# Kernel tuning notes

Hardware: AMD Instinct MI355X
Metric: run time of the kernel (lower is better)

## Reference

```python
import jax, jax.numpy as jnp
import numpy as np

C = 512  # n_channels

def _maxpool2x2(t):
    # t: [B, C, H, W] -> [B, C, H//2, W//2]
    B, Cc, H, W = t.shape
    return t.reshape(B, Cc, H // 2, 2, W // 2, 2).max(axis=(3, 5))

def setup_inputs() -> dict:
    key = jax.random.key(0)
    ks = jax.random.split(key, 6)
    B, H, W = 16, 64, 64
    x = jax.random.normal(ks[0], (B, C, H, W), dtype=jnp.float32)
    # 1x1 conv weights (spectral-normalized convs, no bias) stored as [out, in]
    wq = jax.random.normal(ks[1], (C // 8, C), dtype=jnp.float32) * 0.05
    wk = jax.random.normal(ks[2], (C // 8, C), dtype=jnp.float32) * 0.05
    wv = jax.random.normal(ks[3], (C // 2, C), dtype=jnp.float32) * 0.05
    wo = jax.random.normal(ks[4], (C, C // 2), dtype=jnp.float32) * 0.05
    gamma = jnp.zeros((1,), dtype=jnp.float32) + 0.5  # nonzero so output depends on attention path
    return {"x": x, "wq": wq, "wk": wk, "wv": wv, "wo": wo, "gamma": gamma}

def reference(x, wq, wk, wv, wo, gamma):
    B, Cc, H, W = x.shape
    n = H * W
    # 1x1 convs are channel-mixing matmuls
    f = jnp.einsum('oc,bchw->bohw', wq, x).reshape(B, Cc // 8, n)            # [B, C/8, n]
    g = _maxpool2x2(jnp.einsum('oc,bchw->bohw', wk, x)).reshape(B, Cc // 8, n // 4)  # [B, C/8, n/4]
    h = _maxpool2x2(jnp.einsum('oc,bchw->bohw', wv, x)).reshape(B, Cc // 2, n // 4)  # [B, C/2, n/4]
    # attention: softmax over pooled kv positions
    beta = jax.nn.softmax(jnp.einsum('bcn,bcm->bnm', f, g), axis=-1)         # [B, n, n/4]
    o = jnp.einsum('bcm,bnm->bcn', h, beta).reshape(B, Cc // 2, H, W)        # [B, C/2, H, W]
    o = jnp.einsum('oc,bchw->bohw', wo, o)                                   # [B, C, H, W]
    return gamma.reshape(()) * o + x
```

## Files before the change

kernel.cpp:

```cpp
#include <hip/hip_runtime.h>
#include <cstdint>
#include <cstddef>

namespace {

constexpr int kB  = 16;
constexpr int kC  = 512;
constexpr int kCQ = 64;
constexpr int kCV = 256;
constexpr int kN  = 4096;
constexpr int kM  = 1024;

typedef _Float16 f16;
typedef _Float16 f16x8 __attribute__((ext_vector_type(8)));
typedef float    f32x4 __attribute__((ext_vector_type(4)));

__global__ __launch_bounds__(256)
void convert_weights_kernel(const float* __restrict__ wq,
                            const float* __restrict__ wk,
                            const float* __restrict__ wv,
                            const float* __restrict__ wo,
                            const float* __restrict__ gamma,
                            f16* __restrict__ wcat,
                            f16* __restrict__ woh)
{
    const int idx = blockIdx.x * 256 + threadIdx.x;
    if (idx < 49152) {
        const int e = idx * 4;
        const int r = e >> 9, c = e & 511;
        const float* src = (r < 64)  ? (wq + ((size_t)r << 9))
                         : (r < 128) ? (wk + ((size_t)(r - 64) << 9))
                                     : (wv + ((size_t)(r - 128) << 9));
        float4 v = *(const float4*)(src + c);
        union { f16 h4[4]; uint2 u; } pk;
        pk.h4[0] = (f16)v.x;
        pk.h4[1] = (f16)v.y;
        pk.h4[2] = (f16)v.z;
        pk.h4[3] = (f16)v.w;
        *(uint2*)(wcat + e) = pk.u;
    } else {
        const int e = (idx - 49152) * 4;
        const float g = gamma[0];
        float4 v = *(const float4*)(wo + e);
        union { f16 h4[4]; uint2 u; } pk;
        pk.h4[0] = (f16)(g * v.x);
        pk.h4[1] = (f16)(g * v.y);
        pk.h4[2] = (f16)(g * v.z);
        pk.h4[3] = (f16)(g * v.w);
        *(uint2*)(woh + e) = pk.u;
    }
}

__global__ __launch_bounds__(512, 2)
void proj_pool_mfma(const float* __restrict__ x,
                    const f16* __restrict__ wcat,
                    f16* __restrict__ fT,
                    f16* __restrict__ gT,
                    f16* __restrict__ h)
{
    const int nt  = blockIdx.x;
    const int b   = blockIdx.y;
    const int tid = threadIdx.x;
    const int w    = tid >> 6;
    const int lane = tid & 63;
    const int quad = lane >> 4;
    const int lq   = lane & 15;
    const int wr   = w >> 1;
    const int wc   = w & 1;

    __shared__ alignas(16) f16 As[384 * 40];
    __shared__ alignas(16) f16 Bs[128 * 40];

    const float* Xb = x + (size_t)b * kC * kN + nt * 128;

    f32x4 acc[6][4];
#pragma unroll
    for (int i = 0; i < 6; ++i)
#pragma unroll
        for (int j = 0; j < 4; ++j) acc[i][j] = {0.f, 0.f, 0.f, 0.f};

    const int bn = tid & 127;
    const int kg = tid >> 7;

    uint4 pa[3];
    float xv[8];
#pragma unroll
    for (int p = 0; p < 3; ++p) {
        const int unit = tid + p * 512;
        const int row = unit >> 2, su = unit & 3;
        pa[p] = *(const uint4*)(wcat + (size_t)row * kC + su * 8);
    }
#pragma unroll
    for (int j = 0; j < 8; ++j) xv[j] = Xb[(size_t)(kg * 8 + j) * kN + bn];

    for (int ks = 0; ks < 16; ++ks) {
        __syncthreads();
#pragma unroll
        for (int p = 0; p < 3; ++p) {
            const int unit = tid + p * 512;
            const int row = unit >> 2, su = unit & 3;
            *(uint4*)&As[row * 40 + su * 8] = pa[p];
        }
        {
            union { f16 hh[8]; uint4 u; } pk;
#pragma unroll
            for (int j = 0; j < 8; ++j) pk.hh[j] = (f16)xv[j];
            *(uint4*)&Bs[bn * 40 + kg * 8] = pk.u;
        }
        __syncthreads();
        if (ks < 15) {
            const int k0 = (ks + 1) * 32;
#pragma unroll
            for (int p = 0; p < 3; ++p) {
                const int unit = tid + p * 512;
                const int row = unit >> 2, su = unit & 3;
                pa[p] = *(const uint4*)(wcat + (size_t)row * kC + k0 + su * 8);
            }
#pragma unroll
            for (int j = 0; j < 8; ++j)
                xv[j] = Xb[(size_t)(k0 + kg * 8 + j) * kN + bn];
        }

        f16x8 bsv[4];
#pragma unroll
        for (int tj = 0; tj < 4; ++tj) {
            const int col = (tj < 2) ? (wc * 32 + tj * 16 + lq)
                                     : (64 + wc * 32 + (tj - 2) * 16 + lq);
            bsv[tj] = *(const f16x8*)&Bs[col * 40 + quad * 8];
        }
        __builtin_amdgcn_s_setprio(1);
#pragma unroll
        for (int ti = 0; ti < 6; ++ti) {
            const f16x8 af = *(const f16x8*)&As[(wr * 96 + ti * 16 + lq) * 40 + quad * 8];
#pragma unroll
            for (int tj = 0; tj < 4; ++tj)
                acc[ti][tj] = __builtin_amdgcn_mfma_f32_16x16x32_f16(
                    af, bsv[tj], acc[ti][tj], 0, 0, 0);
        }
        __builtin_amdgcn_s_setprio(0);
    }

#pragma unroll
    for (int ti = 0; ti < 6; ++ti) {
        const int ch0 = wr * 96 + ti * 16;
        if (ch0 < 64) {
            f16* fb = fT + (size_t)b * kN * kCQ;
#pragma unroll
            for (int tj = 0; tj < 4; ++tj) {
                const int col = (tj < 2) ? (wc * 32 + tj * 16 + lq)
                                         : (64 + wc * 32 + (tj - 2) * 16 + lq);
                const int n = nt * 128 + col;
                union { f16 h4[4]; uint2 u; } pk;
#pragma unroll
                for (int r = 0; r < 4; ++r) pk.h4[r] = (f16)acc[ti][tj][r];
                *(uint2*)(fb + (size_t)n * kCQ + ch0 + quad * 4) = pk.u;
            }
        } else {
#pragma unroll
            for (int tjp = 0; tjp < 2; ++tjp) {
                float p[4];
#pragma unroll
                for (int r = 0; r < 4; ++r) {
                    float v = fmaxf(acc[ti][tjp][r], acc[ti][tjp + 2][r]);
                    v = fmaxf(v, __shfl_xor(v, 1, 64));
                    p[r] = v;
                }
                const int m = nt * 32 + wc * 16 + tjp * 8 + (lq >> 1);
                if ((lq & 1) == 0) {
                    if (ch0 < 128) {
                        union { f16 h4[4]; uint2 u; } pk;
#pragma unroll
                        for (int r = 0; r < 4; ++r) pk.h4[r] = (f16)p[r];
                        *(uint2*)(gT + ((size_t)b * kM + m) * kCQ + (ch0 - 64) + quad * 4) = pk.u;
                    } else {
#pragma unroll
                        for (int r = 0; r < 4; ++r) {
                            const int ch = ch0 - 128 + quad * 4 + r;
                            h[((size_t)b * kCV + ch) * kM + m] = (f16)p[r];
                        }
                    }
                }
            }
        }
    }
}

__global__ __launch_bounds__(256, 2)
void attn_out_kernel(const f16* __restrict__ fT,
                     const f16* __restrict__ gT,
                     const f16* __restrict__ hmat,
                     const f16* __restrict__ woh,
                     const float* __restrict__ x,
                     float* __restrict__ out)
{
    const int qt   = blockIdx.x;
    const int b    = blockIdx.y;
    const int tid  = threadIdx.x;
    const int w    = tid >> 6;
    const int lane = tid & 63;
    const int quad = lane >> 4;
    const int lq   = lane & 15;

    __shared__ union alignas(16) SMem {
        struct {
            f16   fsT[128 * 72];
            f16   gsT[32 * 64];
            f16   hs[256 * 40];
            f16   ps[64 * 40];
        } p1;
        struct {
            f16 osT[64 * 264];
            f16 wos[256 * 40];
        } p2;
    } sm;

    {
        const f16* fb = fT + ((size_t)b * kN + qt * 128) * kCQ;
#pragma unroll
        for (int p = 0; p < 4; ++p) {
            const int unit = tid + p * 256;
            const int q = unit >> 3, u = unit & 7;
            *(uint4*)&sm.p1.fsT[q * 72 + u * 8] = *(const uint4*)(fb + q * 64 + u * 8);
        }
    }
    __syncthreads();

    const f16x8 afA0 = *(const f16x8*)&sm.p1.fsT[(w * 16 + lq) * 72 + quad * 8];
    const f16x8 afA1 = *(const f16x8*)&sm.p1.fsT[(w * 16 + lq) * 72 + 32 + quad * 8];
    const f16x8 afB0 = *(const f16x8*)&sm.p1.fsT[(64 + w * 16 + lq) * 72 + quad * 8];
    const f16x8 afB1 = *(const f16x8*)&sm.p1.fsT[(64 + w * 16 + lq) * 72 + 32 + quad * 8];

    float mA = -3.0e38f, lA = 0.f, mB = -3.0e38f, lB = 0.f;
    f32x4 o_accA[16], o_accB[16];
#pragma unroll
    for (int ci = 0; ci < 16; ++ci) {
        o_accA[ci] = {0.f, 0.f, 0.f, 0.f};
        o_accB[ci] = {0.f, 0.f, 0.f, 0.f};
    }

    const f16* gTb = gT + (size_t)b * kM * kCQ;
    const f16* hb  = hmat + (size_t)b * kCV * kM;

    const int gm = tid >> 3, gsu = tid & 7, ggu = gsu ^ (gm & 7);
    const int hc = tid >> 2, hu = tid & 3;
    uint4 pg, ph[4];
    {
        pg = *(const uint4*)(gTb + (size_t)gm * kCQ + ggu * 8);
#pragma unroll
        for (int p = 0; p < 4; ++p)
            ph[p] = *(const uint4*)(hb + (size_t)(hc + p * 64) * kM + hu * 8);
    }

    for (int mi = 0; mi < 32; ++mi) {
        __syncthreads();
        *(uint4*)&sm.p1.gsT[gm * 64 + gsu * 8] = pg;
#pragma unroll
        for (int p = 0; p < 4; ++p)
            *(uint4*)&sm.p1.hs[(hc + p * 64) * 40 + hu * 8] = ph[p];
        __syncthreads();
        if (mi < 31) {
            const int m1 = (mi + 1) * 32;
            pg = *(const uint4*)(gTb + (size_t)(m1 + gm) * kCQ + ggu * 8);
#pragma unroll
            for (int p = 0; p < 4; ++p)
                ph[p] = *(const uint4*)(hb + (size_t)(hc + p * 64) * kM + m1 + hu * 8);
        }

        const int mr0 = lq, mr1 = 16 + lq;
        const f16x8 bg00 = *(const f16x8*)&sm.p1.gsT[mr0 * 64 + ((quad)     ^ (mr0 & 7)) * 8];
        const f16x8 bg01 = *(const f16x8*)&sm.p1.gsT[mr0 * 64 + ((4 + quad) ^ (mr0 & 7)) * 8];
        const f16x8 bg10 = *(const f16x8*)&sm.p1.gsT[mr1 * 64 + ((quad)     ^ (mr1 & 7)) * 8];
        const f16x8 bg11 = *(const f16x8*)&sm.p1.gsT[mr1 * 64 + ((4 + quad) ^ (mr1 & 7)) * 8];
        f32x4 s0A = {0.f,0.f,0.f,0.f}, s1A = {0.f,0.f,0.f,0.f};
        f32x4 s0B = {0.f,0.f,0.f,0.f}, s1B = {0.f,0.f,0.f,0.f};
        s0A = __builtin_amdgcn_mfma_f32_16x16x32_f16(bg00, afA0, s0A, 0, 0, 0);
        s0A = __builtin_amdgcn_mfma_f32_16x16x32_f16(bg01, afA1, s0A, 0, 0, 0);
        s1A = __builtin_amdgcn_mfma_f32_16x16x32_f16(bg10, afA0, s1A, 0, 0, 0);
        s1A = __builtin_amdgcn_mfma_f32_16x16x32_f16(bg11, afA1, s1A, 0, 0, 0);
        s0B = __builtin_amdgcn_mfma_f32_16x16x32_f16(bg00, afB0, s0B, 0, 0, 0);
        s0B = __builtin_amdgcn_mfma_f32_16x16x32_f16(bg01, afB1, s0B, 0, 0, 0);
        s1B = __builtin_amdgcn_mfma_f32_16x16x32_f16(bg10, afB0, s1B, 0, 0, 0);
        s1B = __builtin_amdgcn_mfma_f32_16x16x32_f16(bg11, afB1, s1B, 0, 0, 0);

        float alA;
        {
            float cm = fmaxf(fmaxf(fmaxf(s0A[0], s0A[1]), fmaxf(s0A[2], s0A[3])),
                             fmaxf(fmaxf(s1A[0], s1A[1]), fmaxf(s1A[2], s1A[3])));
            cm = fmaxf(cm, __shfl_xor(cm, 16, 64));
            cm = fmaxf(cm, __shfl_xor(cm, 32, 64));
            const float nm = fmaxf(mA, cm);
            alA = __expf(mA - nm);
            float e0[4], e1[4];
#pragma unroll
            for (int r = 0; r < 4; ++r) { e0[r] = __expf(s0A[r] - nm); e1[r] = __expf(s1A[r] - nm); }
            float psum = (e0[0]+e0[1])+(e0[2]+e0[3])+(e1[0]+e1[1])+(e1[2]+e1[3]);
            psum += __shfl_xor(psum, 16, 64);
            psum += __shfl_xor(psum, 32, 64);
            mA = nm;
            lA = lA * alA + psum;
            union { f16 h4[4]; uint2 u; } pk0, pk1;
#pragma unroll
            for (int r = 0; r < 4; ++r) { pk0.h4[r] = (f16)e0[r]; pk1.h4[r] = (f16)e1[r]; }
            *(uint2*)&sm.p1.ps[(w * 16 + lq) * 40 + quad * 4]      = pk0.u;
            *(uint2*)&sm.p1.ps[(w * 16 + lq) * 40 + 16 + quad * 4] = pk1.u;
        }
        const f16x8 bpA = *(const f16x8*)&sm.p1.ps[(w * 16 + lq) * 40 + quad * 8];
        __builtin_amdgcn_sched_barrier(0);

        float alB;
        {
            float cm = fmaxf(fmaxf(fmaxf(s0B[0], s0B[1]), fmaxf(s0B[2], s0B[3])),
                             fmaxf(fmaxf(s1B[0], s1B[1]), fmaxf(s1B[2], s1B[3])));
            cm = fmaxf(cm, __shfl_xor(cm, 16, 64));
            cm = fmaxf(cm, __shfl_xor(cm, 32, 64));
            const float nm = fmaxf(mB, cm);
            alB = __expf(mB - nm);
            float e0[4], e1[4];
#pragma unroll
            for (int r = 0; r < 4; ++r) { e0[r] = __expf(s0B[r] - nm); e1[r] = __expf(s1B[r] - nm); }
            float psum = (e0[0]+e0[1])+(e0[2]+e0[3])+(e1[0]+e1[1])+(e1[2]+e1[3]);
            psum += __shfl_xor(psum, 16, 64);
            psum += __shfl_xor(psum, 32, 64);
            mB = nm;
            lB = lB * alB + psum;
            union { f16 h4[4]; uint2 u; } pk0, pk1;
#pragma unroll
            for (int r = 0; r < 4; ++r) { pk0.h4[r] = (f16)e0[r]; pk1.h4[r] = (f16)e1[r]; }
            *(uint2*)&sm.p1.ps[(w * 16 + lq) * 40 + quad * 4]      = pk0.u;
            *(uint2*)&sm.p1.ps[(w * 16 + lq) * 40 + 16 + quad * 4] = pk1.u;
        }
        const f16x8 bpB = *(const f16x8*)&sm.p1.ps[(w * 16 + lq) * 40 + quad * 8];
        __builtin_amdgcn_sched_barrier(0);

        __builtin_amdgcn_s_setprio(1);
#pragma unroll
        for (int ci = 0; ci < 16; ++ci) {
            const f16x8 ha = *(const f16x8*)&sm.p1.hs[(ci * 16 + lq) * 40 + quad * 8];
            o_accA[ci] *= alA;
            o_accA[ci] = __builtin_amdgcn_mfma_f32_16x16x32_f16(ha, bpA, o_accA[ci], 0, 0, 0);
            o_accB[ci] *= alB;
            o_accB[ci] = __builtin_amdgcn_mfma_f32_16x16x32_f16(ha, bpB, o_accB[ci], 0, 0, 0);
        }
        __builtin_amdgcn_s_setprio(0);
    }

    const float invA = 1.0f / lA;
    const float invB = 1.0f / lB;

    const int woc = tid >> 2, wu = tid & 3;
    uint4 pw[4];
#pragma unroll
    for (int p = 0; p < 4; ++p)
        pw[p] = *(const uint4*)(woh + (size_t)(woc + p * 64) * 256 + wu * 8);

    __syncthreads();

#pragma unroll
    for (int ci = 0; ci < 16; ++ci) {
        union { f16 h4[4]; uint2 u; } pk;
#pragma unroll
        for (int r = 0; r < 4; ++r) pk.h4[r] = (f16)(o_accA[ci][r] * invA);
        *(uint2*)&sm.p2.osT[(w * 16 + lq) * 264 + ci * 16 + quad * 4] = pk.u;
    }

    int s = 0;
    for (int tile = 0; tile < 2; ++tile) {
        for (int half = 0; half < 2; ++half) {
            f32x4 acc2[16];
#pragma unroll
            for (int os = 0; os < 16; ++os) acc2[os] = {0.f, 0.f, 0.f, 0.f};

            for (int ck = 0; ck < 8; ++ck) {
                __syncthreads();
#pragma unroll
                for (int p = 0; p < 4; ++p)
                    *(uint4*)&sm.p2.wos[(woc + p * 64) * 40 + wu * 8] = pw[p];
                __syncthreads();
                ++s;
                if (s < 32) {
                    const int sp = s & 15;
#pragma unroll
                    for (int p = 0; p < 4; ++p)
                        pw[p] = *(const uint4*)(woh +
                            (size_t)((sp >> 3) * 256 + woc + p * 64) * 256 +
                            (sp & 7) * 32 + wu * 8);
                }
                const f16x8 bo = *(const f16x8*)&sm.p2.osT[(w * 16 + lq) * 264 + ck * 32 + quad * 8];
                __builtin_amdgcn_s_setprio(1);
#pragma unroll
                for (int os = 0; os < 16; ++os) {
                    const f16x8 wa = *(const f16x8*)&sm.p2.wos[(os * 16 + lq) * 40 + quad * 8];
                    acc2[os] = __builtin_amdgcn_mfma_f32_16x16x32_f16(wa, bo, acc2[os], 0, 0, 0);
                }
                __builtin_amdgcn_s_setprio(0);
            }

            const int n0 = qt * 128 + tile * 64 + w * 16 + lq;
#pragma unroll
            for (int os = 0; os < 16; ++os) {
#pragma unroll
                for (int r = 0; r < 4; ++r) {
                    const int oc = half * 256 + os * 16 + quad * 4 + r;
                    const size_t idx = ((size_t)b * kC + oc) * (size_t)kN + n0;
                    out[idx] = acc2[os][r] + x[idx];
                }
            }
        }
        if (tile == 0) {
#pragma unroll
            for (int ci = 0; ci < 16; ++ci) {
                union { f16 h4[4]; uint2 u; } pk;
#pragma unroll
                for (int r = 0; r < 4; ++r) pk.h4[r] = (f16)(o_accB[ci][r] * invB);
                *(uint2*)&sm.p2.osT[(w * 16 + lq) * 264 + ci * 16 + quad * 4] = pk.u;
            }
        }
    }
}

}

extern "C" void kernel_launch(void* const* d_in, const int* in_sizes, int n_in,
                              void* d_out, int out_size, void* d_ws, size_t ws_size,
                              hipStream_t stream) {
    const float* x     = (const float*)d_in[0];
    const float* wq    = (const float*)d_in[1];
    const float* wk    = (const float*)d_in[2];
    const float* wv    = (const float*)d_in[3];
    const float* wo    = (const float*)d_in[4];
    const float* gamma = (const float*)d_in[5];
    float* out = (float*)d_out;

    f16* fT   = (f16*)d_ws;
    f16* gT   = fT  + (size_t)kB * kN * kCQ;
    f16* hw   = gT  + (size_t)kB * kM * kCQ;
    f16* woh  = hw  + (size_t)kB * kCV * kM;
    f16* wcat = woh + (size_t)kC * kCV;

    hipLaunchKernelGGL(convert_weights_kernel, dim3(320), dim3(256), 0, stream,
                       wq, wk, wv, wo, gamma, wcat, woh);
    hipLaunchKernelGGL(proj_pool_mfma, dim3(32, kB), dim3(512), 0, stream,
                       x, wcat, fT, gT, hw);
    hipLaunchKernelGGL(attn_out_kernel, dim3(32, kB), dim3(256), 0, stream,
                       fT, gT, hw, woh, x, out);
}
```

Baseline: 472.3 us.

## Double-buffer LDS stages and split projection channels across a grid dimension

The projection kernel now splits its 384 output channels into two 192-channel blocks along a new grid dimension. It reads weight fragments straight from global memory into registers instead of through LDS, and double-buffers the X tile so each k-step needs only one barrier. The attention kernel double-buffers the g/h chunks and the output-weight tiles with a two-deep register prefetch, which halves the barriers per iteration. In exchange, the X tile is converted twice (once per channel block), LDS use in the attention kernel grows, and register pressure may rise.

```diff
diff --git a/kernel.cpp b/kernel.cpp
--- a/kernel.cpp
+++ b/kernel.cpp
@@ -33,25 +33,21 @@
                                      : (wv + ((size_t)(r - 128) << 9));
         float4 v = *(const float4*)(src + c);
         union { f16 h4[4]; uint2 u; } pk;
-        pk.h4[0] = (f16)v.x;
-        pk.h4[1] = (f16)v.y;
-        pk.h4[2] = (f16)v.z;
-        pk.h4[3] = (f16)v.w;
+        pk.h4[0] = (f16)v.x; pk.h4[1] = (f16)v.y;
+        pk.h4[2] = (f16)v.z; pk.h4[3] = (f16)v.w;
         *(uint2*)(wcat + e) = pk.u;
     } else {
         const int e = (idx - 49152) * 4;
         const float g = gamma[0];
         float4 v = *(const float4*)(wo + e);
         union { f16 h4[4]; uint2 u; } pk;
-        pk.h4[0] = (f16)(g * v.x);
-        pk.h4[1] = (f16)(g * v.y);
-        pk.h4[2] = (f16)(g * v.z);
-        pk.h4[3] = (f16)(g * v.w);
+        pk.h4[0] = (f16)(g * v.x); pk.h4[1] = (f16)(g * v.y);
+        pk.h4[2] = (f16)(g * v.z); pk.h4[3] = (f16)(g * v.w);
         *(uint2*)(woh + e) = pk.u;
     }
 }
 
-__global__ __launch_bounds__(512, 2)
+__global__ __launch_bounds__(512, 4)
 void proj_pool_mfma(const float* __restrict__ x,
                     const f16* __restrict__ wcat,
                     f16* __restrict__ fT,
@@ -59,7 +55,8 @@
                     f16* __restrict__ h)
 {
     const int nt  = blockIdx.x;
-    const int b   = blockIdx.y;
+    const int mt  = blockIdx.y;
+    const int b   = blockIdx.z;
     const int tid = threadIdx.x;
     const int w    = tid >> 6;
     const int lane = tid & 63;
@@ -68,57 +65,56 @@
     const int wr   = w >> 1;
     const int wc   = w & 1;
 
-    __shared__ alignas(16) f16 As[384 * 40];
-    __shared__ alignas(16) f16 Bs[128 * 40];
-
+    __shared__ alignas(16) f16 Bs[2][128 * 36];
+
+    const f16*   Ab = wcat + (size_t)mt * 192 * kC;
     const float* Xb = x + (size_t)b * kC * kN + nt * 128;
 
-    f32x4 acc[6][4];
-#pragma unroll
-    for (int i = 0; i < 6; ++i)
+    f32x4 acc[3][4];
+#pragma unroll
+    for (int i = 0; i < 3; ++i)
 #pragma unroll
         for (int j = 0; j < 4; ++j) acc[i][j] = {0.f, 0.f, 0.f, 0.f};
 
     const int bn = tid & 127;
     const int kg = tid >> 7;
-
-    uint4 pa[3];
     float xv[8];
-#pragma unroll
-    for (int p = 0; p < 3; ++p) {
-        const int unit = tid + p * 512;
-        const int row = unit >> 2, su = unit & 3;
-        pa[p] = *(const uint4*)(wcat + (size_t)row * kC + su * 8);
-    }
-#pragma unroll
-    for (int j = 0; j < 8; ++j) xv[j] = Xb[(size_t)(kg * 8 + j) * kN + bn];
+
+    auto loadB = [&](int k0) {
+#pragma unroll
+        for (int j = 0; j < 8; ++j) xv[j] = Xb[(size_t)(k0 + kg * 8 + j) * kN + bn];
+    };
+    auto writeB = [&](int buf) {
+        union { f16 hh[8]; uint4 u; } pk;
+#pragma unroll
+        for (int j = 0; j < 8; ++j) pk.hh[j] = (f16)xv[j];
+        *(uint4*)&Bs[buf][bn * 36 + kg * 8] = pk.u;
+    };
+
+    const f16* arow[3];
+#pragma unroll
+    for (int ti = 0; ti < 3; ++ti)
+        arow[ti] = Ab + (size_t)(wr * 48 + ti * 16 + lq) * kC + quad * 8;
+
+    f16x8 afp[3];
+#pragma unroll
+    for (int ti = 0; ti < 3; ++ti) afp[ti] = *(const f16x8*)(arow[ti]);
+
+    loadB(0);
+    writeB(0);
+    __syncthreads();
 
     for (int ks = 0; ks < 16; ++ks) {
-        __syncthreads();
-#pragma unroll
-        for (int p = 0; p < 3; ++p) {
-            const int unit = tid + p * 512;
-            const int row = unit >> 2, su = unit & 3;
-            *(uint4*)&As[row * 40 + su * 8] = pa[p];
-        }
-        {
-            union { f16 hh[8]; uint4 u; } pk;
-#pragma unroll
-            for (int j = 0; j < 8; ++j) pk.hh[j] = (f16)xv[j];
-            *(uint4*)&Bs[bn * 40 + kg * 8] = pk.u;
-        }
-        __syncthreads();
+        const int cur = ks & 1;
+        if (ks < 15) loadB((ks + 1) * 32);
+
+        f16x8 afc[3];
+#pragma unroll
+        for (int ti = 0; ti < 3; ++ti) afc[ti] = afp[ti];
         if (ks < 15) {
-            const int k0 = (ks + 1) * 32;
-#pragma unroll
-            for (int p = 0; p < 3; ++p) {
-                const int unit = tid + p * 512;
-                const int row = unit >> 2, su = unit & 3;
-                pa[p] = *(const uint4*)(wcat + (size_t)row * kC + k0 + su * 8);
-            }
-#pragma unroll
-            for (int j = 0; j < 8; ++j)
-                xv[j] = Xb[(size_t)(k0 + kg * 8 + j) * kN + bn];
+#pragma unroll
+            for (int ti = 0; ti < 3; ++ti)
+                afp[ti] = *(const f16x8*)(arow[ti] + (ks + 1) * 32);
         }
 
         f16x8 bsv[4];
@@ -126,23 +122,24 @@
         for (int tj = 0; tj < 4; ++tj) {
             const int col = (tj < 2) ? (wc * 32 + tj * 16 + lq)
                                      : (64 + wc * 32 + (tj - 2) * 16 + lq);
-            bsv[tj] = *(const f16x8*)&Bs[col * 40 + quad * 8];
+            bsv[tj] = *(const f16x8*)&Bs[cur][col * 36 + quad * 8];
         }
         __builtin_amdgcn_s_setprio(1);
 #pragma unroll
-        for (int ti = 0; ti < 6; ++ti) {
-            const f16x8 af = *(const f16x8*)&As[(wr * 96 + ti * 16 + lq) * 40 + quad * 8];
+        for (int ti = 0; ti < 3; ++ti)
 #pragma unroll
             for (int tj = 0; tj < 4; ++tj)
                 acc[ti][tj] = __builtin_amdgcn_mfma_f32_16x16x32_f16(
-                    af, bsv[tj], acc[ti][tj], 0, 0, 0);
-        }
+                    afc[ti], bsv[tj], acc[ti][tj], 0, 0, 0);
         __builtin_amdgcn_s_setprio(0);
-    }
-
-#pragma unroll
-    for (int ti = 0; ti < 6; ++ti) {
-        const int ch0 = wr * 96 + ti * 16;
+
+        if (ks < 15) writeB(cur ^ 1);
+        __syncthreads();
+    }
+
+#pragma unroll
+    for (int ti = 0; ti < 3; ++ti) {
+        const int ch0 = mt * 192 + wr * 48 + ti * 16;
         if (ch0 < 64) {
             f16* fb = fT + (size_t)b * kN * kCQ;
 #pragma unroll
@@ -203,14 +200,14 @@
 
     __shared__ union alignas(16) SMem {
         struct {
-            f16   fsT[128 * 72];
-            f16   gsT[32 * 64];
-            f16   hs[256 * 40];
-            f16   ps[64 * 40];
+            f16 fsT[128 * 72];
+            f16 gsT[2][32 * 64];
+            f16 hs[2][256 * 40];
+            f16 ps[64 * 40];
         } p1;
         struct {
             f16 osT[64 * 264];
-            f16 wos[256 * 40];
+            f16 wos[2][256 * 40];
         } p2;
     } sm;
 
@@ -244,33 +241,35 @@
     const int gm = tid >> 3, gsu = tid & 7, ggu = gsu ^ (gm & 7);
     const int hc = tid >> 2, hu = tid & 3;
     uint4 pg, ph[4];
-    {
-        pg = *(const uint4*)(gTb + (size_t)gm * kCQ + ggu * 8);
+    auto load_chunk = [&](int m0) {
+        pg = *(const uint4*)(gTb + (size_t)(m0 + gm) * kCQ + ggu * 8);
 #pragma unroll
         for (int p = 0; p < 4; ++p)
-            ph[p] = *(const uint4*)(hb + (size_t)(hc + p * 64) * kM + hu * 8);
-    }
+            ph[p] = *(const uint4*)(hb + (size_t)(hc + p * 64) * kM + m0 + hu * 8);
+    };
+    auto write_chunk = [&](int buf) {
+        *(uint4*)&sm.p1.gsT[buf][gm * 64 + gsu * 8] = pg;
+#pragma unroll
+        for (int p = 0; p < 4; ++p)
+            *(uint4*)&sm.p1.hs[buf][(hc + p * 64) * 40 + hu * 8] = ph[p];
+    };
+
+    load_chunk(0);
+    write_chunk(0);
+    load_chunk(32);
+    __syncthreads();
 
     for (int mi = 0; mi < 32; ++mi) {
-        __syncthreads();
-        *(uint4*)&sm.p1.gsT[gm * 64 + gsu * 8] = pg;
-#pragma unroll
-        for (int p = 0; p < 4; ++p)
-            *(uint4*)&sm.p1.hs[(hc + p * 64) * 40 + hu * 8] = ph[p];
-        __syncthreads();
-        if (mi < 31) {
-            const int m1 = (mi + 1) * 32;
-            pg = *(const uint4*)(gTb + (size_t)(m1 + gm) * kCQ + ggu * 8);
-#pragma unroll
-            for (int p = 0; p < 4; ++p)
-                ph[p] = *(const uint4*)(hb + (size_t)(hc + p * 64) * kM + m1 + hu * 8);
-        }
+        const int cur = mi & 1;
+        if (mi < 31) write_chunk(cur ^ 1);
+        if (mi < 30) load_chunk((mi + 2) * 32);
 
         const int mr0 = lq, mr1 = 16 + lq;
-        const f16x8 bg00 = *(const f16x8*)&sm.p1.gsT[mr0 * 64 + ((quad)     ^ (mr0 & 7)) * 8];
-        const f16x8 bg01 = *(const f16x8*)&sm.p1.gsT[mr0 * 64 + ((4 + quad) ^ (mr0 & 7)) * 8];
-        const f16x8 bg10 = *(const f16x8*)&sm.p1.gsT[mr1 * 64 + ((quad)     ^ (mr1 & 7)) * 8];
-        const f16x8 bg11 = *(const f16x8*)&sm.p1.gsT[mr1 * 64 + ((4 + quad) ^ (mr1 & 7)) * 8];
+        const f16* gsc = &sm.p1.gsT[cur][0];
+        const f16x8 bg00 = *(const f16x8*)&gsc[mr0 * 64 + ((quad       ^ (mr0 & 7)) * 8)];
+        const f16x8 bg01 = *(const f16x8*)&gsc[mr0 * 64 + (((4 + quad) ^ (mr0 & 7)) * 8)];
+        const f16x8 bg10 = *(const f16x8*)&gsc[mr1 * 64 + ((quad       ^ (mr1 & 7)) * 8)];
+        const f16x8 bg11 = *(const f16x8*)&gsc[mr1 * 64 + (((4 + quad) ^ (mr1 & 7)) * 8)];
         f32x4 s0A = {0.f,0.f,0.f,0.f}, s1A = {0.f,0.f,0.f,0.f};
         f32x4 s0B = {0.f,0.f,0.f,0.f}, s1B = {0.f,0.f,0.f,0.f};
         s0A = __builtin_amdgcn_mfma_f32_16x16x32_f16(bg00, afA0, s0A, 0, 0, 0);
@@ -335,35 +334,47 @@
         __builtin_amdgcn_s_setprio(1);
 #pragma unroll
         for (int ci = 0; ci < 16; ++ci) {
-            const f16x8 ha = *(const f16x8*)&sm.p1.hs[(ci * 16 + lq) * 40 + quad * 8];
+            const f16x8 ha = *(const f16x8*)&sm.p1.hs[cur][(ci * 16 + lq) * 40 + quad * 8];
             o_accA[ci] *= alA;
             o_accA[ci] = __builtin_amdgcn_mfma_f32_16x16x32_f16(ha, bpA, o_accA[ci], 0, 0, 0);
             o_accB[ci] *= alB;
             o_accB[ci] = __builtin_amdgcn_mfma_f32_16x16x32_f16(ha, bpB, o_accB[ci], 0, 0, 0);
         }
         __builtin_amdgcn_s_setprio(0);
+
+        __syncthreads();
     }
 
     const float invA = 1.0f / lA;
     const float invB = 1.0f / lB;
 
+#pragma unroll
+    for (int ci = 0; ci < 16; ++ci) {
+        union { f16 h4[4]; uint2 u; } pk;
+#pragma unroll
+        for (int r = 0; r < 4; ++r) pk.h4[r] = (f16)(o_accA[ci][r] * invA);
+        *(uint2*)&sm.p2.osT[(w * 16 + lq) * 264 + ci * 16 + quad * 4] = pk.u;
+    }
+
     const int woc = tid >> 2, wu = tid & 3;
     uint4 pw[4];
-#pragma unroll
-    for (int p = 0; p < 4; ++p)
-        pw[p] = *(const uint4*)(woh + (size_t)(woc + p * 64) * 256 + wu * 8);
-
+    auto load_w = [&](int sp) {
+#pragma unroll
+        for (int p = 0; p < 4; ++p)
+            pw[p] = *(const uint4*)(woh +
+                (size_t)((sp >> 3) * 256 + woc + p * 64) * 256 + (sp & 7) * 32 + wu * 8);
+    };
+    auto write_w = [&](int buf) {
+#pragma unroll
+        for (int p = 0; p < 4; ++p)
+            *(uint4*)&sm.p2.wos[buf][(woc + p * 64) * 40 + wu * 8] = pw[p];
+    };
+
+    load_w(0);
+    write_w(0);
+    load_w(1);
     __syncthreads();
 
-#pragma unroll
-    for (int ci = 0; ci < 16; ++ci) {
-        union { f16 h4[4]; uint2 u; } pk;
-#pragma unroll
-        for (int r = 0; r < 4; ++r) pk.h4[r] = (f16)(o_accA[ci][r] * invA);
-        *(uint2*)&sm.p2.osT[(w * 16 + lq) * 264 + ci * 16 + quad * 4] = pk.u;
-    }
-
-    int s = 0;
     for (int tile = 0; tile < 2; ++tile) {
         for (int half = 0; half < 2; ++half) {
             f32x4 acc2[16];
@@ -371,28 +382,20 @@
             for (int os = 0; os < 16; ++os) acc2[os] = {0.f, 0.f, 0.f, 0.f};
 
             for (int ck = 0; ck < 8; ++ck) {
-                __syncthreads();
-#pragma unroll
-                for (int p = 0; p < 4; ++p)
-                    *(uint4*)&sm.p2.wos[(woc + p * 64) * 40 + wu * 8] = pw[p];
-                __syncthreads();
-                ++s;
-                if (s < 32) {
-                    const int sp = s & 15;
-#pragma unroll
-                    for (int p = 0; p < 4; ++p)
-                        pw[p] = *(const uint4*)(woh +
-                            (size_t)((sp >> 3) * 256 + woc + p * 64) * 256 +
-                            (sp & 7) * 32 + wu * 8);
-                }
+                const int sidx = tile * 16 + half * 8 + ck;
+                const int cur2 = sidx & 1;
+                if (sidx < 31) write_w(cur2 ^ 1);
+                if (sidx < 30) load_w((sidx + 2) & 15);
+
                 const f16x8 bo = *(const f16x8*)&sm.p2.osT[(w * 16 + lq) * 264 + ck * 32 + quad * 8];
                 __builtin_amdgcn_s_setprio(1);
 #pragma unroll
                 for (int os = 0; os < 16; ++os) {
-                    const f16x8 wa = *(const f16x8*)&sm.p2.wos[(os * 16 + lq) * 40 + quad * 8];
+                    const f16x8 wa = *(const f16x8*)&sm.p2.wos[cur2][(os * 16 + lq) * 40 + quad * 8];
                     acc2[os] = __builtin_amdgcn_mfma_f32_16x16x32_f16(wa, bo, acc2[os], 0, 0, 0);
                 }
                 __builtin_amdgcn_s_setprio(0);
+                __syncthreads();
             }
 
             const int n0 = qt * 128 + tile * 64 + w * 16 + lq;
@@ -439,7 +442,7 @@
 
     hipLaunchKernelGGL(convert_weights_kernel, dim3(320), dim3(256), 0, stream,
                        wq, wk, wv, wo, gamma, wcat, woh);
-    hipLaunchKernelGGL(proj_pool_mfma, dim3(32, kB), dim3(512), 0, stream,
+    hipLaunchKernelGGL(proj_pool_mfma, dim3(32, 2, kB), dim3(512), 0, stream,
                        x, wcat, fT, gT, hw);
     hipLaunchKernelGGL(attn_out_kernel, dim3(32, kB), dim3(256), 0, stream,
                        fT, gT, hw, woh, x, out);
```

After: 437.4 us. -7.4%, faster.
